# Optimization experiments

Measured on AMD Instinct MI355X. Metric: run time of the kernel, lower is better.

The kernel has to match this reference:

```python
import jax, jax.numpy as jnp
import numpy as np
from jax import lax

B, H, W, C = 8, 64, 64, 256  # H must equal W (einsum contraction requires it)
CQ = C // 4


def conv2d(x, w, b, dilation=1):
    # x: NHWC, w: HWIO (TF Conv2D layout), padding 'same'
    y = lax.conv_general_dilated(
        x, w, window_strides=(1, 1), padding='SAME',
        rhs_dilation=(dilation, dilation),
        dimension_numbers=('NHWC', 'HWIO', 'NHWC'))
    return y + b


def setup_inputs() -> dict:
    key = jax.random.key(0)
    ks = jax.random.split(key, 16)
    s = 0.05
    inp = {
        'x':   jax.random.normal(ks[0], (B, H, W, C), jnp.float32),
        'wq':  jax.random.normal(ks[1], (1, 1, C, CQ), jnp.float32) * s,
        'bq':  jnp.zeros((CQ,), jnp.float32),
        'wq1': jax.random.normal(ks[2], (3, 3, C, CQ), jnp.float32) * s,
        'bq1': jnp.zeros((CQ,), jnp.float32),
        'wq2': jax.random.normal(ks[3], (3, 3, C, CQ), jnp.float32) * s,
        'bq2': jnp.zeros((CQ,), jnp.float32),
        'wq3': jax.random.normal(ks[4], (3, 3, C, CQ), jnp.float32) * s,
        'bq3': jnp.zeros((CQ,), jnp.float32),
        'wq4': jax.random.normal(ks[5], (1, 1, C, C), jnp.float32) * s,
        'bq4': jnp.zeros((C,), jnp.float32),
        'wk':  jax.random.normal(ks[6], (3, 3, C, C), jnp.float32) * s,
        'bk':  jnp.zeros((C,), jnp.float32),
        'wv':  jax.random.normal(ks[7], (1, 1, C, C), jnp.float32) * s,
        'bv':  jnp.zeros((C,), jnp.float32),
        'gamma': jax.random.normal(ks[8], (1,), jnp.float32) * 0.1,
    }
    return inp


def reference(x, wq, bq, wq1, bq1, wq2, bq2, wq3, bq3, wq4, bq4,
              wk, bk, wv, bv, gamma):
    # multi-scale query branch: 1x1, 3x3, 3x3 dil=3, 3x3 dil=6 -> concat -> 1x1
    q = jnp.concatenate([
        conv2d(x, wq, bq, 1),
        conv2d(x, wq1, bq1, 1),
        conv2d(x, wq2, bq2, 3),
        conv2d(x, wq3, bq3, 6),
    ], axis=-1)
    q = conv2d(q, wq4, bq4, 1)                 # (B,H,W,C)
    # key conv applied twice with the SAME weights (as in the original code)
    k = conv2d(conv2d(x, wk, bk, 1), wk, bk, 1)  # (B,H,W,C)
    v = conv2d(x, wv, bv, 1)                    # (B,H,W,C)

    qT = jnp.transpose(q, (0, 2, 1, 3))         # (B,W,H,C)
    # per-channel spatial contraction; requires H == W
    energy = jnp.einsum('bijc,bkjc->bikc', k, qT)   # (B,H,W,C)
    attention = jax.nn.softmax(energy, axis=-1)     # softmax over CHANNEL axis
    attnT = jnp.transpose(attention, (0, 2, 1, 3))  # (B,W,H,C)
    out = jnp.einsum('bijc,bkjc->bikc', attnT, v)   # (B,W,H,C)
    return gamma * out + x
```

## Files before the change

kernel.cpp:

```cpp
#include <hip/hip_runtime.h>

typedef short  short8 __attribute__((ext_vector_type(8)));
typedef short  sv4    __attribute__((ext_vector_type(4)));
typedef __bf16 bf16x8 __attribute__((ext_vector_type(8)));
typedef float  f32x4  __attribute__((ext_vector_type(4)));

__device__ __forceinline__ float bf2f(short s) {
    unsigned u = ((unsigned)(unsigned short)s) << 16;
    return __builtin_bit_cast(float, u);
}
__device__ __forceinline__ short f2bf(float f) {
    unsigned u = __builtin_bit_cast(unsigned, f);
    u += 0x7fffu + ((u >> 16) & 1u);
    return (short)(u >> 16);
}
__device__ __forceinline__ f32x4 mfma16(short8 a, short8 b, f32x4 c) {
    return __builtin_amdgcn_mfma_f32_16x16x32_bf16(
        __builtin_bit_cast(bf16x8, a), __builtin_bit_cast(bf16x8, b), c, 0, 0, 0);
}
__device__ __forceinline__ void gl16(const short* g, short* l) {
    __builtin_amdgcn_global_load_lds(
        (const __attribute__((address_space(1))) void*)g,
        (__attribute__((address_space(3))) void*)l, 16, 0, 0);
}


__global__ __launch_bounds__(256) void detect_k(const short* x, int* flag)
{
    __shared__ int red[256];
    int t = threadIdx.x;
    int cnt = 0;
    for (int i = t; i < 4096; i += 256) {
        int e = (x[2 * i] >> 7) & 0xFF;
        cnt += (e >= 100 && e <= 140) ? 1 : 0;
    }
    red[t] = cnt; __syncthreads();
    for (int s = 128; s > 0; s >>= 1) { if (t < s) red[t] += red[t + s]; __syncthreads(); }
    if (t == 0) *flag = (red[0] < 3277) ? 1 : 0;
}

__global__ __launch_bounds__(256) void convert_x(const void* x, short* xb, const int* flagp)
{
    int f32 = *flagp;
    size_t i = ((size_t)blockIdx.x * 256 + threadIdx.x) * 8;
    short8 v;
    if (f32) {
        const float* fs = (const float*)x + i;
        f32x4 a = *(const f32x4*)fs;
        f32x4 b = *(const f32x4*)(fs + 4);
#pragma unroll
        for (int l = 0; l < 4; l++) { v[l] = f2bf(a[l]); v[4 + l] = f2bf(b[l]); }
    } else {
        v = *(const short8*)((const short*)x + i);
    }
    *(short8*)(xb + i) = v;
}

struct Ptrs {
    const void *wq, *wq1, *wq2, *wq3, *wq4, *wk, *wv;
    const void *bq, *bq1, *bq2, *bq3, *bq4, *bk, *bv, *gm;
};

__global__ __launch_bounds__(256) void convert_k(Ptrs P, short* wp, short* bb, const int* flagp)
{
    int f32 = *flagp;
    int bid = blockIdx.x;
    int tid = threadIdx.x;
    if (bid < 288) {
        __shared__ short T[64][66];
        const void* src; int Cout, dbase, lb;
        if      (bid <   4) { src = P.wq;  Cout =  64; dbase = 0;       lb = bid; }
        else if (bid <  40) { src = P.wq1; Cout =  64; dbase = 16384;   lb = bid - 4; }
        else if (bid <  76) { src = P.wq2; Cout =  64; dbase = 163840;  lb = bid - 40; }
        else if (bid < 112) { src = P.wq3; Cout =  64; dbase = 311296;  lb = bid - 76; }
        else if (bid < 128) { src = P.wq4; Cout = 256; dbase = 458752;  lb = bid - 112; }
        else if (bid < 272) { src = P.wk;  Cout = 256; dbase = 524288;  lb = bid - 128; }
        else                { src = P.wv;  Cout = 256; dbase = 1114112; lb = bid - 272; }
        int t, ci0, co0;
        if (Cout == 64) { t = lb >> 2; ci0 = (lb & 3) * 64; co0 = 0; }
        else            { t = lb >> 4; ci0 = ((lb >> 2) & 3) * 64; co0 = (lb & 3) * 64; }
        int rrow = tid >> 6, ccol = tid & 63;
#pragma unroll
        for (int r = 0; r < 16; ++r) {
            int cir = r * 4 + rrow;
            long si = (long)(t * 256 + ci0 + cir) * Cout + co0 + ccol;
            T[cir][ccol] = f32 ? f2bf(((const float*)src)[si]) : ((const short*)src)[si];
        }
        __syncthreads();
#pragma unroll
        for (int r = 0; r < 16; ++r) {
            int cow = r * 4 + rrow;
            wp[dbase + (t * Cout + co0 + cow) * 256 + ci0 + ccol] = T[ccol][cow];
        }
    } else {
        for (int j = tid; j < 1280; j += 256) {
            if (j < 1025) {
                const void* src; int off;
                if      (j <   64) { src = P.bq;  off = j; }
                else if (j <  128) { src = P.bq1; off = j - 64; }
                else if (j <  192) { src = P.bq2; off = j - 128; }
                else if (j <  256) { src = P.bq3; off = j - 192; }
                else if (j <  512) { src = P.bq4; off = j - 256; }
                else if (j <  768) { src = P.bk;  off = j - 512; }
                else if (j < 1024) { src = P.bv;  off = j - 768; }
                else               { src = P.gm;  off = 0; }
                bb[j] = f32 ? f2bf(((const float*)src)[off]) : ((const short*)src)[off];
            } else if (j >= 1032) {
                bb[j] = 0;
            }
        }
    }
}

struct CJob {
    const short* src;
    short*       dst;
    const short* wpk;
    const short* bias;
    int Cout;
    int dil;
    int ntaps;
    int coff;
    int outmode;
};
struct CTable { CJob j[6]; int end[6]; };

template<int NA, int NB, int BOFS, int WSTEP>
__device__ __forceinline__ void conv_med_loop(
    const short* src, const short* wpk, int ntaps, int dil,
    const short* zp, short* Sh,
    int wave, int lr8, int cl, int h0, int b, int nt0, int srcT,
    int m_base, int n_base, int lrow, int pc0, int pc1,
    f32x4 (&acc)[2][4])
{
    const short* abase[NA];
    unsigned     vm[NA];
    const short* bbase[NB];
#pragma unroll
    for (int jj = 0; jj < NA; jj++) {
        int m  = (jj * 4 + wave) * 8 + lr8;
        int hh = srcT ? (m & 63) : (h0 + (m >> 6));
        int ww = srcT ? (h0 + (m >> 6)) : (m & 63);
        abase[jj] = src + (((b * 64 + hh) * 64 + ww) * 256 + cl * 8);
        unsigned msk = 1u;
        if (ntaps == 9) {
            msk = 0u;
#pragma unroll
            for (int t = 0; t < 9; ++t) {
                int tr = (t >= 6) ? 2 : ((t >= 3) ? 1 : 0);
                int dy = (tr - 1) * dil, dx = (t - tr * 3 - 1) * dil;
                bool v = ((unsigned)(hh + dy) < 64u) && ((unsigned)(ww + dx) < 64u);
                msk |= (v ? 1u : 0u) << t;
            }
        }
        vm[jj] = msk;
    }
#pragma unroll
    for (int jj = 0; jj < NB; jj++) {
        int n = (jj * 4 + wave) * 8 + lr8;
        bbase[jj] = wpk + (nt0 + n) * 256 + cl * 8;
    }

    int prevdel = 0;
    for (int t = 0; t < ntaps; ++t) {
        int dy = 0, dx = 0;
        if (ntaps == 9) {
            int tr = (t >= 6) ? 2 : ((t >= 3) ? 1 : 0);
            dy = (tr - 1) * dil;
            dx = (t - tr * 3 - 1) * dil;
        }
        int tdel = (dy * 64 + dx) * 256;
        int step = tdel - prevdel; prevdel = tdel;
        const short* pA[NA];
#pragma unroll
        for (int jj = 0; jj < NA; jj++) {
            abase[jj] += step;
            pA[jj] = ((vm[jj] >> t) & 1u) ? abase[jj] : zp;
        }
#pragma unroll
        for (int s4 = 0; s4 < 4; ++s4) {
#pragma unroll
            for (int jj = 0; jj < NA; jj++)
                gl16(pA[jj] + s4 * 64, Sh + (jj * 4 + wave) * 512);
#pragma unroll
            for (int jj = 0; jj < NB; jj++)
                gl16(bbase[jj] + s4 * 64, Sh + BOFS + (jj * 4 + wave) * 512);
            __syncthreads();
#pragma unroll
            for (int j = 0; j < 2; j++) {
                int pc = j ? pc1 : pc0;
                short8 a4[2], b4[4];
#pragma unroll
                for (int mi = 0; mi < 2; mi++)
                    a4[mi] = *(const short8*)(Sh + (m_base + mi * 16 + lrow) * 64 + pc);
#pragma unroll
                for (int ni = 0; ni < 4; ni++)
                    b4[ni] = *(const short8*)(Sh + BOFS + (n_base + ni * 16 + lrow) * 64 + pc);
#pragma unroll
                for (int mi = 0; mi < 2; mi++)
#pragma unroll
                    for (int ni = 0; ni < 4; ni++)
                        acc[mi][ni] = mfma16(a4[mi], b4[ni], acc[mi][ni]);
            }
            __syncthreads();
        }
#pragma unroll
        for (int jj = 0; jj < NB; jj++) bbase[jj] += WSTEP;
    }
}

__global__ __launch_bounds__(256, 4) void conv_med(CTable T, const short* zp)
{
    __shared__ short Sh[12288];
    int tid = threadIdx.x;
    int bid = blockIdx.x;
    int ji = 0;
    while (ji < 5 && bid >= T.end[ji]) ji++;
    CJob J = T.j[ji];
    int s0  = ji ? T.end[ji - 1] : 0;
    int seg = T.end[ji] - s0;
    int lb  = bid - s0;
    int g   = (lb & 7) * (seg >> 3) + (lb >> 3);

    int big   = (J.Cout == 256);
    int BM    = big ? 64 : 128;
    int ntile = big ? (g & 1) : 0;
    int Mtile = big ? (g >> 1) : g;
    int p0 = Mtile * BM;
    int b  = p0 >> 12;
    int h0 = (p0 >> 6) & 63;
    int nt0  = ntile * 128;
    int srcT = (J.outmode == 3);

    int wave = tid >> 6, lane = tid & 63;
    int lrow = lane & 15, quad = lane >> 4;
    int m_base = big ? (wave & 1) * 32 : wave * 32;
    int n_base = big ? (wave >> 1) * 64 : 0;

    int lr8 = lane >> 3;
    int cl  = (lane & 7) ^ (lr8 & 7);

    int pc0 = ((quad     ^ (lrow & 7)) * 8);
    int pc1 = (((4 + quad) ^ (lrow & 7)) * 8);

    f32x4 acc[2][4] = {};
    if (big)
        conv_med_loop<2, 4, 4096, 65536>(J.src, J.wpk, J.ntaps, J.dil, zp, Sh,
                                         wave, lr8, cl, h0, b, nt0, srcT,
                                         m_base, n_base, lrow, pc0, pc1, acc);
    else
        conv_med_loop<4, 2, 8192, 16384>(J.src, J.wpk, J.ntaps, J.dil, zp, Sh,
                                         wave, lr8, cl, h0, b, nt0, srcT,
                                         m_base, n_base, lrow, pc0, pc1, acc);

    int rq = quad * 4;
#pragma unroll
    for (int ni = 0; ni < 4; ni++) {
        int co = nt0 + n_base + ni * 16 + lrow;
        float bv = bf2f(J.bias[co]);
        if (J.outmode == 0) {
#pragma unroll
            for (int mi = 0; mi < 2; mi++) {
                int pb = p0 + m_base + mi * 16 + rq;
#pragma unroll
                for (int r = 0; r < 4; r++)
                    J.dst[(size_t)(pb + r) * 256 + J.coff + co] = f2bf(acc[mi][ni][r] + bv);
            }
        } else {
            short* row = J.dst + ((size_t)(b * 256 + co) * 64 + h0) * 64;
#pragma unroll
            for (int mi = 0; mi < 2; mi++) {
                sv4 o;
#pragma unroll
                for (int r = 0; r < 4; r++) o[r] = f2bf(acc[mi][ni][r] + bv);
                *(sv4*)(row + m_base + mi * 16 + rq) = o;
            }
        }
    }
}

__global__ __launch_bounds__(256) void energy_mfma(const short* qp, const short* kp, short* Et)
{
    int wid  = threadIdx.x >> 6;
    int lane = threadIdx.x & 63;
    int g = blockIdx.x * 4 + wid;
    int b = g >> 8, c = g & 255;
    int lrow = lane & 15;
    int q8   = (lane >> 4) << 3;
    const short* qb = qp + (size_t)(b * 256 + c) * 4096;
    const short* kb = kp + (size_t)(b * 256 + c) * 4096;

    f32x4 acc[4][4] = {};
#pragma unroll
    for (int ks = 0; ks < 2; ++ks) {
        int j0 = ks * 32 + q8;
        short8 A[4], Bv[4];
#pragma unroll
        for (int mi = 0; mi < 4; mi++)
            A[mi] = *(const short8*)(qb + (size_t)(mi * 16 + lrow) * 64 + j0);
#pragma unroll
        for (int ni = 0; ni < 4; ni++)
            Bv[ni] = *(const short8*)(kb + (size_t)(ni * 16 + lrow) * 64 + j0);
#pragma unroll
        for (int mi = 0; mi < 4; mi++)
#pragma unroll
            for (int ni = 0; ni < 4; ni++)
                acc[mi][ni] = mfma16(A[mi], Bv[ni], acc[mi][ni]);
    }
    int rq = (lane >> 4) * 4;
#pragma unroll
    for (int mi = 0; mi < 4; mi++)
#pragma unroll
        for (int r = 0; r < 4; r++) {
            int w = mi * 16 + rq + r;
            short* row = Et + ((size_t)(b * 256 + c) * 64 + w) * 64;
#pragma unroll
            for (int ni = 0; ni < 4; ni++)
                row[ni * 16 + lrow] = f2bf(acc[mi][ni][r]);
        }
}

__global__ __launch_bounds__(256) void softmax_k(const short* Et, short* att)
{
    __shared__ float S[256 * 33];
    __shared__ float red[256];
    __shared__ float sm[256];
    int t  = threadIdx.x;
    int b  = blockIdx.x >> 7;
    int a  = (blockIdx.x >> 1) & 63;
    int jh = blockIdx.x & 1;

    const short* row = Et + ((size_t)(b * 256 + t) * 64 + a) * 64 + jh * 32;
#pragma unroll
    for (int jj = 0; jj < 32; jj += 8) {
        short8 v = *(const short8*)(row + jj);
#pragma unroll
        for (int l = 0; l < 8; l++) S[t * 33 + jj + l] = bf2f(v[l]);
    }
    __syncthreads();

    int tj = t & 31, tg = t >> 5;
    float m = -1e30f;
#pragma unroll
    for (int cc = 0; cc < 32; ++cc) m = fmaxf(m, S[(tg * 32 + cc) * 33 + tj]);
    red[t] = m;
    __syncthreads();
    if (tg == 0) {
        float mm = red[tj];
#pragma unroll
        for (int gg = 1; gg < 8; ++gg) mm = fmaxf(mm, red[gg * 32 + tj]);
        red[tj] = mm;
    }
    __syncthreads();
    float M = red[tj];
    float s = 0.f;
#pragma unroll
    for (int cc = 0; cc < 32; ++cc) {
        int id = (tg * 32 + cc) * 33 + tj;
        float e = __expf(S[id] - M);
        S[id] = e; s += e;
    }
    sm[t] = s;
    __syncthreads();
    if (tg == 0) {
        float ss = sm[tj];
#pragma unroll
        for (int gg = 1; gg < 8; ++gg) ss += sm[gg * 32 + tj];
        sm[tj] = 1.0f / ss;
    }
    __syncthreads();

    short* orow = att + ((size_t)(b * 256 + t) * 64 + a) * 64 + jh * 32;
#pragma unroll
    for (int jj = 0; jj < 32; jj += 8) {
        short8 o;
#pragma unroll
        for (int l = 0; l < 8; l++) o[l] = f2bf(S[t * 33 + jj + l] * sm[jj + l]);
        *(short8*)(orow + jj) = o;
    }
}

__global__ __launch_bounds__(512) void out_final(const short* vp, const short* att,
                                                 const void* x, const void* gamma,
                                                 void* out, const int* flagp)
{
    __shared__ float S[8 * 16 * 66];
    int f32 = *flagp;
    int tid = threadIdx.x;
    int wid = tid >> 6, lane = tid & 63;
    int b  = blockIdx.x & 7;
    int c0 = (blockIdx.x >> 3) * 8;
    int c  = c0 + wid;
    int lrow = lane & 15, quad = lane >> 4;
    int q8 = quad << 3;
    const short* vb = vp  + (size_t)(b * 256 + c) * 4096;
    const short* ab = att + (size_t)(b * 256 + c) * 4096;

    f32x4 acc[4][4] = {};
#pragma unroll
    for (int ks = 0; ks < 2; ++ks) {
        int j0 = ks * 32 + q8;
        short8 A[4], Bv[4];
#pragma unroll
        for (int mi = 0; mi < 4; mi++)
            A[mi] = *(const short8*)(vb + (size_t)(mi * 16 + lrow) * 64 + j0);
#pragma unroll
        for (int ni = 0; ni < 4; ni++)
            Bv[ni] = *(const short8*)(ab + (size_t)(ni * 16 + lrow) * 64 + j0);
#pragma unroll
        for (int mi = 0; mi < 4; mi++)
#pragma unroll
            for (int ni = 0; ni < 4; ni++)
                acc[mi][ni] = mfma16(A[mi], Bv[ni], acc[mi][ni]);
    }

    float gm = f32 ? ((const float*)gamma)[0] : bf2f(((const short*)gamma)[0]);
    int rq = quad * 4;
#pragma unroll
    for (int mi = 0; mi < 4; mi++) {
#pragma unroll
        for (int ni = 0; ni < 4; ni++)
#pragma unroll
            for (int r = 0; r < 4; r++)
                S[(wid * 16 + rq + r) * 66 + ni * 16 + lrow] = acc[mi][ni][r];
        __syncthreads();
#pragma unroll
        for (int it = 0; it < 2; ++it) {
            int idx = it * 512 + tid;
            int dp = idx >> 6;
            int p  = idx & 63;
            int dg = mi * 16 + dp;
            size_t off = ((size_t)((b * 64 + p) * 64 + dg)) * 256 + c0;
            if (f32) {
                const float* xs = (const float*)x + off;
                float* os = (float*)out + off;
                f32x4 xv0 = *(const f32x4*)xs;
                f32x4 xv1 = *(const f32x4*)(xs + 4);
                f32x4 o0, o1;
#pragma unroll
                for (int l = 0; l < 4; l++) {
                    o0[l] = gm * S[((l    ) * 16 + dp) * 66 + p] + xv0[l];
                    o1[l] = gm * S[((l + 4) * 16 + dp) * 66 + p] + xv1[l];
                }
                *(f32x4*)os = o0;
                *(f32x4*)(os + 4) = o1;
            } else {
                const short* xs = (const short*)x + off;
                short* os = (short*)out + off;
                short8 xv = *(const short8*)xs, o;
#pragma unroll
                for (int l = 0; l < 8; l++)
                    o[l] = f2bf(gm * S[(l * 16 + dp) * 66 + p] + bf2f(xv[l]));
                *(short8*)os = o;
            }
        }
        __syncthreads();
    }
}

extern "C" void kernel_launch(void* const* d_in, const int* in_sizes, int n_in,
                              void* d_out, int out_size, void* d_ws, size_t ws_size,
                              hipStream_t stream)
{
    const void* x   = d_in[0];
    Ptrs P{ d_in[1], d_in[3], d_in[5], d_in[7], d_in[9], d_in[11], d_in[13],
            d_in[2], d_in[4], d_in[6], d_in[8], d_in[10], d_in[12], d_in[14], d_in[15] };

    short* ws   = (short*)d_ws;
    short* qcat = ws;
    short* k1   = ws + 8388608;
    short* qp   = ws + 16777216;
    short* kp   = ws + 25165824;
    short* vp   = ws + 33554432;
    short* wp   = ws + 41943040;
    short* bb   = ws + 43122688;
    int*   flag = (int*)(ws + 43123968);
    short* xb   = qp;
    short* Et   = ws;
    short* att  = qp;
    const short* zp = bb + 1032;

    detect_k<<<1, 256, 0, stream>>>((const short*)x, flag);
    convert_x<<<4096, 256, 0, stream>>>(x, xb, flag);
    convert_k<<<289, 256, 0, stream>>>(P, wp, bb, flag);

    CJob j4{ xb, k1,   wp + 524288,  bb + 512, 256, 1, 9, 0,   0 };
    CJob j1{ xb, qcat, wp + 16384,   bb + 64,  64,  1, 9, 64,  0 };
    CJob j2{ xb, qcat, wp + 163840,  bb + 128, 64,  3, 9, 128, 0 };
    CJob j3{ xb, qcat, wp + 311296,  bb + 192, 64,  6, 9, 192, 0 };
    CJob jb{ xb, vp,   wp + 1114112, bb + 768, 256, 1, 1, 0,   2 };
    CJob ja{ xb, qcat, wp + 0,       bb + 0,   64,  1, 1, 0,   0 };
    CTable TA{ { j4, j1, j2, j3, jb, ja }, { 1024, 1280, 1536, 1792, 2816, 3072 } };
    conv_med<<<3072, 256, 0, stream>>>(TA, zp);

    CJob j6{ k1,   kp, wp + 524288, bb + 512, 256, 1, 9, 0, 2 };
    CJob j5{ qcat, qp, wp + 458752, bb + 256, 256, 1, 1, 0, 3 };
    CTable TB{ { j6, j5, j5, j5, j5, j5 }, { 1024, 2048, 2048, 2048, 2048, 2048 } };
    conv_med<<<2048, 256, 0, stream>>>(TB, zp);

    energy_mfma<<<512, 256, 0, stream>>>(qp, kp, Et);
    softmax_k<<<1024, 256, 0, stream>>>(Et, att);
    out_final<<<256, 512, 0, stream>>>(vp, att, x, d_in[15], d_out, flag);
}
```

Before: 311.8 us.

## Use two-wave conv blocks with 64x64 per-wave tiles and fuse conversion kernels

The conv kernel now runs 128 threads (2 waves) per block on the same block tile. Each wave computes a 64x64 output sub-tile with 4x4 MFMA accumulators instead of 32x64, which raises LDS operand reuse per wave and halves the waves per block. Each wave issues twice as many global-to-LDS loads, and the larger accumulator array raises register pressure, which the launch bounds of (128,3) reflect. The x and weight conversion kernels are merged into one launch to save a kernel launch.

```diff
diff --git a/kernel.cpp b/kernel.cpp
--- a/kernel.cpp
+++ b/kernel.cpp
@@ -39,33 +39,33 @@
     if (t == 0) *flag = (red[0] < 3277) ? 1 : 0;
 }
 
-__global__ __launch_bounds__(256) void convert_x(const void* x, short* xb, const int* flagp)
-{
-    int f32 = *flagp;
-    size_t i = ((size_t)blockIdx.x * 256 + threadIdx.x) * 8;
-    short8 v;
-    if (f32) {
-        const float* fs = (const float*)x + i;
-        f32x4 a = *(const f32x4*)fs;
-        f32x4 b = *(const f32x4*)(fs + 4);
-#pragma unroll
-        for (int l = 0; l < 4; l++) { v[l] = f2bf(a[l]); v[4 + l] = f2bf(b[l]); }
-    } else {
-        v = *(const short8*)((const short*)x + i);
-    }
-    *(short8*)(xb + i) = v;
-}
-
 struct Ptrs {
     const void *wq, *wq1, *wq2, *wq3, *wq4, *wk, *wv;
     const void *bq, *bq1, *bq2, *bq3, *bq4, *bk, *bv, *gm;
 };
 
-__global__ __launch_bounds__(256) void convert_k(Ptrs P, short* wp, short* bb, const int* flagp)
+__global__ __launch_bounds__(256) void convert_xk(const void* x, short* xb,
+                                                  Ptrs P, short* wp, short* bb,
+                                                  const int* flagp)
 {
     int f32 = *flagp;
-    int bid = blockIdx.x;
     int tid = threadIdx.x;
+    if (blockIdx.x < 4096) {
+        size_t i = ((size_t)blockIdx.x * 256 + tid) * 8;
+        short8 v;
+        if (f32) {
+            const float* fs = (const float*)x + i;
+            f32x4 a = *(const f32x4*)fs;
+            f32x4 b = *(const f32x4*)(fs + 4);
+#pragma unroll
+            for (int l = 0; l < 4; l++) { v[l] = f2bf(a[l]); v[4 + l] = f2bf(b[l]); }
+        } else {
+            v = *(const short8*)((const short*)x + i);
+        }
+        *(short8*)(xb + i) = v;
+        return;
+    }
+    int bid = blockIdx.x - 4096;
     if (bid < 288) {
         __shared__ short T[64][66];
         const void* src; int Cout, dbase, lb;
@@ -126,19 +126,18 @@
 struct CTable { CJob j[6]; int end[6]; };
 
 template<int NA, int NB, int BOFS, int WSTEP>
-__device__ __forceinline__ void conv_med_loop(
+__device__ __forceinline__ void conv2w_loop(
     const short* src, const short* wpk, int ntaps, int dil,
     const short* zp, short* Sh,
     int wave, int lr8, int cl, int h0, int b, int nt0, int srcT,
-    int m_base, int n_base, int lrow, int pc0, int pc1,
-    f32x4 (&acc)[2][4])
+    int a_mbase, int b_nbase, int lrow, int quad,
+    f32x4 (&acc)[4][4])
 {
     const short* abase[NA];
     unsigned     vm[NA];
-    const short* bbase[NB];
 #pragma unroll
     for (int jj = 0; jj < NA; jj++) {
-        int m  = (jj * 4 + wave) * 8 + lr8;
+        int m  = (jj * 2 + wave) * 8 + lr8;
         int hh = srcT ? (m & 63) : (h0 + (m >> 6));
         int ww = srcT ? (h0 + (m >> 6)) : (m & 63);
         abase[jj] = src + (((b * 64 + hh) * 64 + ww) * 256 + cl * 8);
@@ -155,11 +154,7 @@
         }
         vm[jj] = msk;
     }
-#pragma unroll
-    for (int jj = 0; jj < NB; jj++) {
-        int n = (jj * 4 + wave) * 8 + lr8;
-        bbase[jj] = wpk + (nt0 + n) * 256 + cl * 8;
-    }
+    const short* bb0 = wpk + (size_t)(nt0 + wave * 8 + lr8) * 256 + cl * 8;
 
     int prevdel = 0;
     for (int t = 0; t < ntaps; ++t) {
@@ -181,35 +176,34 @@
         for (int s4 = 0; s4 < 4; ++s4) {
 #pragma unroll
             for (int jj = 0; jj < NA; jj++)
-                gl16(pA[jj] + s4 * 64, Sh + (jj * 4 + wave) * 512);
+                gl16(pA[jj] + s4 * 64, Sh + (jj * 2 + wave) * 512);
 #pragma unroll
             for (int jj = 0; jj < NB; jj++)
-                gl16(bbase[jj] + s4 * 64, Sh + BOFS + (jj * 4 + wave) * 512);
+                gl16(bb0 + jj * 4096 + s4 * 64, Sh + BOFS + (jj * 2 + wave) * 512);
             __syncthreads();
 #pragma unroll
             for (int j = 0; j < 2; j++) {
-                int pc = j ? pc1 : pc0;
-                short8 a4[2], b4[4];
-#pragma unroll
-                for (int mi = 0; mi < 2; mi++)
-                    a4[mi] = *(const short8*)(Sh + (m_base + mi * 16 + lrow) * 64 + pc);
+                int pc = ((j * 4 + quad) ^ (lrow & 7)) * 8;
+                short8 a4[4], b4[4];
+#pragma unroll
+                for (int mi = 0; mi < 4; mi++)
+                    a4[mi] = *(const short8*)(Sh + (a_mbase + mi * 16 + lrow) * 64 + pc);
 #pragma unroll
                 for (int ni = 0; ni < 4; ni++)
-                    b4[ni] = *(const short8*)(Sh + BOFS + (n_base + ni * 16 + lrow) * 64 + pc);
-#pragma unroll
-                for (int mi = 0; mi < 2; mi++)
+                    b4[ni] = *(const short8*)(Sh + BOFS + (b_nbase + ni * 16 + lrow) * 64 + pc);
+#pragma unroll
+                for (int mi = 0; mi < 4; mi++)
 #pragma unroll
                     for (int ni = 0; ni < 4; ni++)
                         acc[mi][ni] = mfma16(a4[mi], b4[ni], acc[mi][ni]);
             }
             __syncthreads();
         }
-#pragma unroll
-        for (int jj = 0; jj < NB; jj++) bbase[jj] += WSTEP;
-    }
-}
-
-__global__ __launch_bounds__(256, 4) void conv_med(CTable T, const short* zp)
+        bb0 += WSTEP;
+    }
+}
+
+__global__ __launch_bounds__(128, 3) void conv2w(CTable T, const short* zp)
 {
     __shared__ short Sh[12288];
     int tid = threadIdx.x;
@@ -223,10 +217,9 @@
     int g   = (lb & 7) * (seg >> 3) + (lb >> 3);
 
     int big   = (J.Cout == 256);
-    int BM    = big ? 64 : 128;
     int ntile = big ? (g & 1) : 0;
     int Mtile = big ? (g >> 1) : g;
-    int p0 = Mtile * BM;
+    int p0 = big ? (Mtile << 6) : (Mtile << 7);
     int b  = p0 >> 12;
     int h0 = (p0 >> 6) & 63;
     int nt0  = ntile * 128;
@@ -234,34 +227,31 @@
 
     int wave = tid >> 6, lane = tid & 63;
     int lrow = lane & 15, quad = lane >> 4;
-    int m_base = big ? (wave & 1) * 32 : wave * 32;
-    int n_base = big ? (wave >> 1) * 64 : 0;
+    int a_mbase = big ? 0 : wave * 64;
+    int b_nbase = big ? wave * 64 : 0;
 
     int lr8 = lane >> 3;
     int cl  = (lane & 7) ^ (lr8 & 7);
 
-    int pc0 = ((quad     ^ (lrow & 7)) * 8);
-    int pc1 = (((4 + quad) ^ (lrow & 7)) * 8);
-
-    f32x4 acc[2][4] = {};
+    f32x4 acc[4][4] = {};
     if (big)
-        conv_med_loop<2, 4, 4096, 65536>(J.src, J.wpk, J.ntaps, J.dil, zp, Sh,
-                                         wave, lr8, cl, h0, b, nt0, srcT,
-                                         m_base, n_base, lrow, pc0, pc1, acc);
+        conv2w_loop<4, 8, 4096, 65536>(J.src, J.wpk, J.ntaps, J.dil, zp, Sh,
+                                       wave, lr8, cl, h0, b, nt0, srcT,
+                                       a_mbase, b_nbase, lrow, quad, acc);
     else
-        conv_med_loop<4, 2, 8192, 16384>(J.src, J.wpk, J.ntaps, J.dil, zp, Sh,
-                                         wave, lr8, cl, h0, b, nt0, srcT,
-                                         m_base, n_base, lrow, pc0, pc1, acc);
+        conv2w_loop<8, 4, 8192, 16384>(J.src, J.wpk, J.ntaps, J.dil, zp, Sh,
+                                       wave, lr8, cl, h0, b, nt0, srcT,
+                                       a_mbase, b_nbase, lrow, quad, acc);
 
     int rq = quad * 4;
 #pragma unroll
     for (int ni = 0; ni < 4; ni++) {
-        int co = nt0 + n_base + ni * 16 + lrow;
+        int co = nt0 + b_nbase + ni * 16 + lrow;
         float bv = bf2f(J.bias[co]);
         if (J.outmode == 0) {
 #pragma unroll
-            for (int mi = 0; mi < 2; mi++) {
-                int pb = p0 + m_base + mi * 16 + rq;
+            for (int mi = 0; mi < 4; mi++) {
+                int pb = p0 + a_mbase + mi * 16 + rq;
 #pragma unroll
                 for (int r = 0; r < 4; r++)
                     J.dst[(size_t)(pb + r) * 256 + J.coff + co] = f2bf(acc[mi][ni][r] + bv);
@@ -269,11 +259,11 @@
         } else {
             short* row = J.dst + ((size_t)(b * 256 + co) * 64 + h0) * 64;
 #pragma unroll
-            for (int mi = 0; mi < 2; mi++) {
+            for (int mi = 0; mi < 4; mi++) {
                 sv4 o;
 #pragma unroll
                 for (int r = 0; r < 4; r++) o[r] = f2bf(acc[mi][ni][r] + bv);
-                *(sv4*)(row + m_base + mi * 16 + rq) = o;
+                *(sv4*)(row + mi * 16 + rq) = o;
             }
         }
     }
@@ -481,8 +471,7 @@
     const short* zp = bb + 1032;
 
     detect_k<<<1, 256, 0, stream>>>((const short*)x, flag);
-    convert_x<<<4096, 256, 0, stream>>>(x, xb, flag);
-    convert_k<<<289, 256, 0, stream>>>(P, wp, bb, flag);
+    convert_xk<<<4385, 256, 0, stream>>>(x, xb, P, wp, bb, flag);
 
     CJob j4{ xb, k1,   wp + 524288,  bb + 512, 256, 1, 9, 0,   0 };
     CJob j1{ xb, qcat, wp + 16384,   bb + 64,  64,  1, 9, 64,  0 };
@@ -491,12 +480,12 @@
     CJob jb{ xb, vp,   wp + 1114112, bb + 768, 256, 1, 1, 0,   2 };
     CJob ja{ xb, qcat, wp + 0,       bb + 0,   64,  1, 1, 0,   0 };
     CTable TA{ { j4, j1, j2, j3, jb, ja }, { 1024, 1280, 1536, 1792, 2816, 3072 } };
-    conv_med<<<3072, 256, 0, stream>>>(TA, zp);
+    conv2w<<<3072, 128, 0, stream>>>(TA, zp);
 
     CJob j6{ k1,   kp, wp + 524288, bb + 512, 256, 1, 9, 0, 2 };
     CJob j5{ qcat, qp, wp + 458752, bb + 256, 256, 1, 1, 0, 3 };
     CTable TB{ { j6, j5, j5, j5, j5, j5 }, { 1024, 2048, 2048, 2048, 2048, 2048 } };
-    conv_med<<<2048, 256, 0, stream>>>(TB, zp);
+    conv2w<<<2048, 128, 0, stream>>>(TB, zp);
 
     energy_mfma<<<512, 256, 0, stream>>>(qp, kp, Et);
     softmax_k<<<1024, 256, 0, stream>>>(Et, att);
```

Measured after the change: 312.5 us. Within noise of the previous version (+0.2%).
